# Optimization experiments

Hardware: AMD Instinct MI355X
Metric: run time of the kernel (lower is better)

The kernel has to match this reference:

```python
import jax, jax.numpy as jnp
import numpy as np
from jax import lax

SCORE_THRESHOLD = 0.02
IOU_THRESHOLD = 0.5
NUM_CLASSES = 80
MAX_DETECTIONS = 10  # tf.image.non_max_suppression max_output_size in the source
ANCHORS = np.array([[1.08, 1.19], [3.42, 4.41], [6.63, 11.38], [9.42, 5.11], [16.62, 10.52]], dtype=np.float32)


def setup_inputs() -> dict:
    key = jax.random.key(0)
    k1, _ = jax.random.split(key)
    B, H, W = 16, 76, 76
    A = ANCHORS.shape[0]
    feats = jax.random.normal(k1, (B, H, W, A * (5 + NUM_CLASSES)), dtype=jnp.float32)
    anchors = jnp.asarray(ANCHORS)
    return {"feats": feats, "anchors": anchors}


def yolo_head(feats, anchors, num_classes):
    """Standard YOLOv2 decode (interpret_prediction)."""
    B, H, W, _ = feats.shape
    A = anchors.shape[0]
    feats = feats.reshape(B, H, W, A, 5 + num_classes)
    gy, gx = jnp.meshgrid(jnp.arange(H), jnp.arange(W), indexing="ij")
    grid = jnp.stack([gx, gy], axis=-1).astype(feats.dtype)  # [H,W,2] in (x,y) order
    conv_dims = jnp.array([W, H], dtype=feats.dtype)
    box_xy = (jax.nn.sigmoid(feats[..., 0:2]) + grid[None, :, :, None, :]) / conv_dims
    box_wh = jnp.exp(feats[..., 2:4]) * anchors[None, None, None, :, :] / conv_dims
    box_confidence = jax.nn.sigmoid(feats[..., 4:5])
    box_class_probs = jax.nn.softmax(feats[..., 5:], axis=-1)
    return box_xy, box_wh, box_confidence, box_class_probs


def _postprocess(feats, anchors):
    box_xy, box_wh, box_confidence, box_class_probs = yolo_head(feats, anchors, NUM_CLASSES)
    box_mins = box_xy - box_wh / 2.0
    box_maxes = box_xy + box_wh / 2.0
    # [y_min, x_min, y_max, x_max] as in the source (indices 1 then 0)
    boxes = jnp.concatenate([box_mins[..., 1:2], box_mins[..., 0:1], box_maxes[..., 1:2], box_maxes[..., 0:1]], axis=-1)
    box_scores = box_confidence * box_class_probs           # [B,H,W,A,C]
    box_classes = jnp.argmax(box_scores, axis=-1)           # [B,H,W,A]
    box_class_scores = jnp.max(box_scores, axis=-1)         # [B,H,W,A]

    # tf.boolean_mask flattens across all dims; emulate with fixed shapes by
    # marking below-threshold candidates as invalid (score -1).
    flat_boxes = boxes.reshape(-1, 4)                       # [N,4]
    flat_scores = box_class_scores.reshape(-1)              # [N]
    flat_classes = box_classes.reshape(-1)                  # [N]
    scores_work = jnp.where(flat_scores >= SCORE_THRESHOLD, flat_scores, -1.0)

    N = flat_boxes.shape[0]
    areas = jnp.maximum(flat_boxes[:, 2] - flat_boxes[:, 0], 0.0) * jnp.maximum(flat_boxes[:, 3] - flat_boxes[:, 1], 0.0)
    idx_range = jnp.arange(N)

    def step(sw, _):
        idx = jnp.argmax(sw)
        s = sw[idx]
        valid = s >= SCORE_THRESHOLD
        box = flat_boxes[idx]                               # [4] = y1,x1,y2,x2
        iy1 = jnp.maximum(box[0], flat_boxes[:, 0])
        ix1 = jnp.maximum(box[1], flat_boxes[:, 1])
        iy2 = jnp.minimum(box[2], flat_boxes[:, 2])
        ix2 = jnp.minimum(box[3], flat_boxes[:, 3])
        inter = jnp.maximum(iy2 - iy1, 0.0) * jnp.maximum(ix2 - ix1, 0.0)
        box_area = jnp.maximum(box[2] - box[0], 0.0) * jnp.maximum(box[3] - box[1], 0.0)
        iou = inter / (box_area + areas - inter + 1e-9)
        suppress = (iou > IOU_THRESHOLD) | (idx_range == idx)
        sw_new = jnp.where(valid & suppress, -1.0, sw)
        row = jnp.concatenate([box, s[None], flat_classes[idx].astype(jnp.float32)[None]])  # [6]
        row = jnp.where(valid, row, jnp.zeros_like(row))
        return sw_new, row

    _, rows = lax.scan(step, scores_work, None, length=MAX_DETECTIONS)
    return rows  # [MAX_DETECTIONS, 6] = [y1,x1,y2,x2,score,class]; zero rows are padding


def reference(feats, anchors):
    return _postprocess(feats, anchors)
```

## Files before the change

kernel.cpp:

```cpp
#include <hip/hip_runtime.h>
#include <stdint.h>

#define N_CAND 462080
#define NBINS  2048
#define HPAD   16
#define HIST_BLOCKS 32
#define COMPACT_BLOCKS 64
#define TARGET 256u
#define SMAX   1024
#define SCORE_THR 0.02f
#define TILEF 2720
#define DB 3610
#define C_CNT 0
#define C_BIN 16
#define C_HD  32
#define C_CD  48


__global__ __launch_bounds__(256) void decode_kernel(
    const float* __restrict__ feats,
    float* __restrict__ scores, unsigned char* __restrict__ cls,
    unsigned int* __restrict__ ctrl, unsigned int* __restrict__ hist)
{
    __shared__ __align__(16) float lds[4 * TILEF];
    const int t = threadIdx.x;
    const int w = t >> 6;
    const int lane = t & 63;
    const int c = lane & 31;
    const int h = lane >> 5;

    if (blockIdx.x == 0) {
        if (t == 0) { ctrl[C_HD] = 0u; ctrl[C_CD] = 0u; }
#pragma unroll
        for (int i = 0; i < 8; ++i) hist[(t * 8 + i) * HPAD] = 0u;
    }

    const int tile = blockIdx.x * 4 + w;
    float* myl = lds + w * TILEF;
    {
        const float4* __restrict__ src = (const float4*)(feats + (size_t)tile * TILEF);
        float4* dst = (float4*)myl;
        float4 v[10];
#pragma unroll
        for (int i = 0; i < 10; ++i) v[i] = src[i * 64 + lane];
        float4 vt;
        if (lane < 40) vt = src[640 + lane];
#pragma unroll
        for (int i = 0; i < 10; ++i) dst[i * 64 + lane] = v[i];
        if (lane < 40) dst[640 + lane] = vt;
    }
    asm volatile("s_waitcnt lgkmcnt(0)" ::: "memory");
    __builtin_amdgcn_sched_barrier(0);

    const float* f = myl + c * 85;
    const int kb = 5 + h * 40;

    float m = f[kb];
    int cb = h * 40;
#pragma unroll
    for (int k = 1; k < 40; ++k) {
        float v = f[kb + k];
        if (v > m) { m = v; cb = h * 40 + k; }
    }
    float mo = __shfl_xor(m, 32);
    int   cbo = __shfl_xor(cb, 32);
    float m0 = (h == 0) ? m : mo,  m1 = (h == 0) ? mo : m;
    int   c0 = (h == 0) ? cb : cbo, c1 = (h == 0) ? cbo : cb;
    float mall = fmaxf(m0, m1);
    int   cls_abs = (m0 >= m1) ? c0 : c1;

    float s0 = 0.f, s1 = 0.f, s2 = 0.f, s3 = 0.f;
#pragma unroll
    for (int k = 0; k < 40; k += 4) {
        s0 += __expf(f[kb + k + 0] - mall);
        s1 += __expf(f[kb + k + 1] - mall);
        s2 += __expf(f[kb + k + 2] - mall);
        s3 += __expf(f[kb + k + 3] - mall);
    }
    float sl = (s0 + s1) + (s2 + s3);
    float sall = sl + __shfl_xor(sl, 32);

    if (h == 0) {
        const int ci = tile * 32 + c;
        float conf = 1.0f / (1.0f + __expf(-f[4]));
        float score = conf / sall;
        scores[ci] = (score >= SCORE_THR) ? score : -1.0f;
        cls[ci] = (unsigned char)cls_abs;
    }
}

__global__ __launch_bounds__(1024) void hist_cutoff_kernel(
    const float* __restrict__ scores, unsigned int* __restrict__ hist,
    unsigned int* __restrict__ ctrl)
{
    __shared__ unsigned int lh[NBINS];
    __shared__ unsigned int pa[1024], pb[1024];
    __shared__ int lastf;
    const int t = threadIdx.x;

    lh[2 * t] = 0u; lh[2 * t + 1] = 0u;
    __syncthreads();

    for (int i = blockIdx.x * 1024 + t; i < N_CAND; i += HIST_BLOCKS * 1024) {
        float s = scores[i];
        if (s >= SCORE_THR) {
            int bin = (int)(s * (float)NBINS);
            bin = bin > (NBINS - 1) ? (NBINS - 1) : bin;
            atomicAdd(&lh[bin], 1u);
        }
    }
    __syncthreads();
    unsigned v0 = lh[2 * t], v1 = lh[2 * t + 1];
    if (v0) atomicAdd(&hist[(2 * t) * HPAD], v0);
    if (v1) atomicAdd(&hist[(2 * t + 1) * HPAD], v1);
    __syncthreads();

    if (t == 0) {
        __threadfence();
        unsigned old = atomicAdd(&ctrl[C_HD], 1u);
        lastf = (old == HIST_BLOCKS - 1) ? 1 : 0;
    }
    __syncthreads();
    if (!lastf) return;
    if (t == 0) __threadfence();
    __syncthreads();

    unsigned b0 = hist[(2 * t) * HPAD];
    unsigned b1 = hist[(2 * t + 1) * HPAD];
    lh[2 * t] = b0; lh[2 * t + 1] = b1;
    pa[t] = b0 + b1;
    __syncthreads();

    unsigned int* srcb = pa; unsigned int* dstb = pb;
    for (int off = 1; off < 1024; off <<= 1) {
        unsigned v = srcb[t] + ((t + off < 1024) ? srcb[t + off] : 0u);
        dstb[t] = v;
        __syncthreads();
        unsigned int* tmp = srcb; srcb = dstb; dstb = tmp;
    }
    unsigned St = srcb[t];
    unsigned Sn = (t < 1023) ? srcb[t + 1] : 0u;

    if (t == 0) {
        ctrl[C_CNT] = 0u;
        if (St < TARGET) ctrl[C_BIN] = 0u;
    }
    if (St >= TARGET && Sn < TARGET) {
        unsigned run = Sn + lh[2 * t + 1];
        ctrl[C_BIN] = (run >= TARGET) ? (unsigned)(2 * t + 1) : (unsigned)(2 * t);
    }
}

__device__ inline float4 decode_box(const float* __restrict__ feats,
                                    const float* __restrict__ anchors, int ci)
{
    int a = ci % 5;
    int cell = ci / 5;
    int gx = cell % 76;
    int gy = (cell / 76) % 76;
    const float* f = feats + (long long)ci * 85;
    float bx = (1.0f / (1.0f + __expf(-f[0])) + (float)gx) / 76.0f;
    float by = (1.0f / (1.0f + __expf(-f[1])) + (float)gy) / 76.0f;
    float bw = __expf(f[2]) * anchors[2 * a]     / 76.0f;
    float bh = __expf(f[3]) * anchors[2 * a + 1] / 76.0f;
    return make_float4(by - bh * 0.5f, bx - bw * 0.5f,
                       by + bh * 0.5f, bx + bw * 0.5f);
}

__global__ __launch_bounds__(1024) void compact_nms_kernel(
    const float* __restrict__ scores, unsigned int* __restrict__ ctrl,
    float* __restrict__ lscore, int* __restrict__ lidx,
    const float* __restrict__ feats, const float* __restrict__ anchors,
    const unsigned char* __restrict__ cls, float* __restrict__ out)
{
    __shared__ unsigned long long wkey[16];
    __shared__ unsigned long long bkey;
    __shared__ float4 bbox;
    __shared__ int lastf;
    const int t = threadIdx.x;

    const int cut = (int)ctrl[C_BIN];
    for (int i = blockIdx.x * 1024 + t; i < N_CAND; i += COMPACT_BLOCKS * 1024) {
        float sw = scores[i];
        if (sw >= SCORE_THR) {
            int bin = (int)(sw * (float)NBINS);
            bin = bin > (NBINS - 1) ? (NBINS - 1) : bin;
            if (bin >= cut) {
                unsigned pos = atomicAdd(&ctrl[C_CNT], 1u);
                if (pos < SMAX) { lscore[pos] = sw; lidx[pos] = i; }
            }
        }
    }
    __syncthreads();
    if (t == 0) {
        __threadfence();
        unsigned old = atomicAdd(&ctrl[C_CD], 1u);
        lastf = (old == COMPACT_BLOCKS - 1) ? 1 : 0;
    }
    __syncthreads();
    if (!lastf) return;
    if (t == 0) __threadfence();
    __syncthreads();

    unsigned cnt = ctrl[C_CNT];
    int n = (cnt < (unsigned)SMAX) ? (int)cnt : SMAX;

    unsigned long long key = 0ull;
    float4 mb = make_float4(0.f, 0.f, 0.f, 0.f);
    float  msc = 0.f, mcls = 0.f;
    unsigned midx = 0xFFFFFFFFu;
    bool aliveb = false;
    if (t < n) {
        msc  = lscore[t];
        midx = (unsigned)lidx[t];
        key  = ((unsigned long long)__float_as_uint(msc) << 32)
             | (unsigned long long)(0xFFFFFFFFu - midx);
        mb   = decode_box(feats, anchors, (int)midx);
        mcls = (float)cls[midx];
        aliveb = true;
    }

    for (int r = 0; r < 10; ++r) {
        unsigned long long k0 = aliveb ? key : 0ull;
#pragma unroll
        for (int msk = 32; msk > 0; msk >>= 1) {
            unsigned long long o = __shfl_xor(k0, msk);
            k0 = (o > k0) ? o : k0;
        }
        if ((t & 63) == 0) wkey[t >> 6] = k0;
        __syncthreads();
        if (t < 16) {
            unsigned long long v = wkey[t];
#pragma unroll
            for (int msk = 8; msk > 0; msk >>= 1) {
                unsigned long long o = __shfl_xor(v, msk);
                v = (o > v) ? o : v;
            }
            if (t == 0) bkey = v;
        }
        __syncthreads();

        unsigned long long wk = bkey;
        bool have = (wk != 0ull);
        unsigned widx = have ? (0xFFFFFFFFu - (unsigned)(wk & 0xFFFFFFFFull)) : 0xFFFFFFFFu;

        if (have && aliveb && midx == widx) {
            bbox = mb;
            out[r * 6 + 0] = mb.x;
            out[r * 6 + 1] = mb.y;
            out[r * 6 + 2] = mb.z;
            out[r * 6 + 3] = mb.w;
            out[r * 6 + 4] = msc;
            out[r * 6 + 5] = mcls;
            aliveb = false;
        }
        if (!have && t == 0) {
#pragma unroll
            for (int q = 0; q < 6; ++q) out[r * 6 + q] = 0.f;
        }
        __syncthreads();

        if (have && aliveb) {
            float4 ab = bbox;
            float aarea = fmaxf(ab.z - ab.x, 0.f) * fmaxf(ab.w - ab.y, 0.f);
            float iy1 = fmaxf(ab.x, mb.x);
            float ix1 = fmaxf(ab.y, mb.y);
            float iy2 = fminf(ab.z, mb.z);
            float ix2 = fminf(ab.w, mb.w);
            float inter = fmaxf(iy2 - iy1, 0.f) * fmaxf(ix2 - ix1, 0.f);
            float carea = fmaxf(mb.z - mb.x, 0.f) * fmaxf(mb.w - mb.y, 0.f);
            float iou = inter / (aarea + carea - inter + 1e-9f);
            if (iou > 0.5f) aliveb = false;
        }
    }
}

extern "C" void kernel_launch(void* const* d_in, const int* in_sizes, int n_in,
                              void* d_out, int out_size, void* d_ws, size_t ws_size,
                              hipStream_t stream) {
    const float* feats   = (const float*)d_in[0];
    const float* anchors = (const float*)d_in[1];
    char* ws = (char*)d_ws;

    unsigned int*   ctrl   = (unsigned int*)(ws + 0);
    unsigned int*   hist   = (unsigned int*)(ws + 256);
    float*          lscore = (float*)(ws + 131328);
    int*            lidx   = (int*)(ws + 135424);
    float*          scores = (float*)(ws + 139520);
    unsigned char*  cls    = (unsigned char*)(ws + 1987840);
    float*          out    = (float*)d_out;

    decode_kernel      <<<DB, 256, 0, stream>>>(feats, scores, cls, ctrl, hist);
    hist_cutoff_kernel <<<HIST_BLOCKS, 1024, 0, stream>>>(scores, hist, ctrl);
    compact_nms_kernel <<<COMPACT_BLOCKS, 1024, 0, stream>>>(scores, ctrl, lscore, lidx,
                                                             feats, anchors, cls, out);
}
```

Measured before the change: 57.88 us.

## Decode candidates with 32-lane groups reading feats directly, dropping LDS staging

The decode kernel now gives each candidate to a 32-lane group. The group reads its 85 floats straight from global memory with coalesced scalar loads, and finds the max, argmax and softmax sum through wave shuffles, in a grid-stride loop over half as many blocks. The previous version staged float4 tiles in LDS and split the 80 classes between two half-waves. The change removes LDS traffic and the staging waits, but scalar loads may pull less memory bandwidth per instruction than float4 loads, and each lane does little useful work per candidate.

```diff
diff --git a/kernel.cpp b/kernel.cpp
--- a/kernel.cpp
+++ b/kernel.cpp
@@ -9,8 +9,8 @@
 #define TARGET 256u
 #define SMAX   1024
 #define SCORE_THR 0.02f
-#define TILEF 2720
-#define DB 3610
+#define DEC_BLOCKS 1805
+#define NGROUPS 14440
 #define C_CNT 0
 #define C_BIN 16
 #define C_HD  32
@@ -22,70 +22,46 @@
     float* __restrict__ scores, unsigned char* __restrict__ cls,
     unsigned int* __restrict__ ctrl, unsigned int* __restrict__ hist)
 {
-    __shared__ __align__(16) float lds[4 * TILEF];
     const int t = threadIdx.x;
-    const int w = t >> 6;
-    const int lane = t & 63;
-    const int c = lane & 31;
-    const int h = lane >> 5;
+    const int l = t & 31;
+    const int gid = blockIdx.x * 8 + (t >> 5);
 
     if (blockIdx.x == 0) {
         if (t == 0) { ctrl[C_HD] = 0u; ctrl[C_CD] = 0u; }
-#pragma unroll
-        for (int i = 0; i < 8; ++i) hist[(t * 8 + i) * HPAD] = 0u;
-    }
-
-    const int tile = blockIdx.x * 4 + w;
-    float* myl = lds + w * TILEF;
-    {
-        const float4* __restrict__ src = (const float4*)(feats + (size_t)tile * TILEF);
-        float4* dst = (float4*)myl;
-        float4 v[10];
-#pragma unroll
-        for (int i = 0; i < 10; ++i) v[i] = src[i * 64 + lane];
-        float4 vt;
-        if (lane < 40) vt = src[640 + lane];
-#pragma unroll
-        for (int i = 0; i < 10; ++i) dst[i * 64 + lane] = v[i];
-        if (lane < 40) dst[640 + lane] = vt;
-    }
-    asm volatile("s_waitcnt lgkmcnt(0)" ::: "memory");
-    __builtin_amdgcn_sched_barrier(0);
-
-    const float* f = myl + c * 85;
-    const int kb = 5 + h * 40;
-
-    float m = f[kb];
-    int cb = h * 40;
-#pragma unroll
-    for (int k = 1; k < 40; ++k) {
-        float v = f[kb + k];
-        if (v > m) { m = v; cb = h * 40 + k; }
-    }
-    float mo = __shfl_xor(m, 32);
-    int   cbo = __shfl_xor(cb, 32);
-    float m0 = (h == 0) ? m : mo,  m1 = (h == 0) ? mo : m;
-    int   c0 = (h == 0) ? cb : cbo, c1 = (h == 0) ? cbo : cb;
-    float mall = fmaxf(m0, m1);
-    int   cls_abs = (m0 >= m1) ? c0 : c1;
-
-    float s0 = 0.f, s1 = 0.f, s2 = 0.f, s3 = 0.f;
-#pragma unroll
-    for (int k = 0; k < 40; k += 4) {
-        s0 += __expf(f[kb + k + 0] - mall);
-        s1 += __expf(f[kb + k + 1] - mall);
-        s2 += __expf(f[kb + k + 2] - mall);
-        s3 += __expf(f[kb + k + 3] - mall);
-    }
-    float sl = (s0 + s1) + (s2 + s3);
-    float sall = sl + __shfl_xor(sl, 32);
-
-    if (h == 0) {
-        const int ci = tile * 32 + c;
-        float conf = 1.0f / (1.0f + __expf(-f[4]));
-        float score = conf / sall;
-        scores[ci] = (score >= SCORE_THR) ? score : -1.0f;
-        cls[ci] = (unsigned char)cls_abs;
+        for (int i = t; i < NBINS; i += 256) hist[i * HPAD] = 0u;
+    }
+
+    for (int ci = gid; ci < N_CAND; ci += NGROUPS) {
+        const float* __restrict__ f = feats + (size_t)ci * 85;
+        float v0 = f[l];
+        float v1 = f[32 + l];
+        float v2 = (l < 21) ? f[64 + l] : 0.f;
+
+        float cv; int cidx;
+        if (l >= 5) { cv = v0; cidx = l - 5; }
+        else        { cv = -3.0e38f; cidx = 0x7fffffff; }
+        if (v1 > cv) { cv = v1; cidx = 27 + l; }
+        if (l < 21 && v2 > cv) { cv = v2; cidx = 59 + l; }
+#pragma unroll
+        for (int m = 16; m; m >>= 1) {
+            float ov = __shfl_xor(cv, m);
+            int   oi = __shfl_xor(cidx, m);
+            if (ov > cv || (ov == cv && oi < cidx)) { cv = ov; cidx = oi; }
+        }
+        const float mall = cv;
+
+        float e = __expf(v1 - mall);
+        if (l >= 5) e += __expf(v0 - mall);
+        if (l < 21) e += __expf(v2 - mall);
+#pragma unroll
+        for (int m = 16; m; m >>= 1) e += __shfl_xor(e, m);
+
+        if (l == 4) {
+            float conf = 1.0f / (1.0f + __expf(-v0));
+            float score = conf / e;
+            scores[ci] = (score >= SCORE_THR) ? score : -1.0f;
+            cls[ci] = (unsigned char)cidx;
+        }
     }
 }
 
@@ -290,7 +266,7 @@
     unsigned char*  cls    = (unsigned char*)(ws + 1987840);
     float*          out    = (float*)d_out;
 
-    decode_kernel      <<<DB, 256, 0, stream>>>(feats, scores, cls, ctrl, hist);
+    decode_kernel      <<<DEC_BLOCKS, 256, 0, stream>>>(feats, scores, cls, ctrl, hist);
     hist_cutoff_kernel <<<HIST_BLOCKS, 1024, 0, stream>>>(scores, hist, ctrl);
     compact_nms_kernel <<<COMPACT_BLOCKS, 1024, 0, stream>>>(scores, ctrl, lscore, lidx,
                                                              feats, anchors, cls, out);
```

Result: slower. 86.35 us (+49.2%).
